# Optimization experiments

Measured on AMD Instinct MI355X. Metric: run time of the kernel, lower is better.

Reference implementation:

```python
import jax, jax.numpy as jnp
import numpy as np


def setup_inputs() -> dict:
    key = jax.random.key(0)
    x = jax.random.normal(key, (8, 192, 64, 64), dtype=jnp.float32)
    return {"x": x}


def reference(x):
    # x: [b, c, h, w]
    b, c, h, w = x.shape
    xf = x.reshape(b, c, h * w)                                   # [b, c, hw]
    # prepend global-mean token -> [b, c, T] with T = hw + 1
    xf = jnp.concatenate([xf.mean(axis=-1, keepdims=True), xf], axis=-1)
    scale = jnp.asarray(c, xf.dtype) ** -0.25                      # 1/sqrt(sqrt(c))
    qs = xf * scale
    # full T x T score matrix, as in the original module
    weight = jnp.einsum('bct,bcs->bts', qs, qs)                    # [b, T, T]
    weight = jax.nn.softmax(weight.astype(jnp.float32), axis=-1).astype(xf.dtype)
    out = jnp.einsum('bts,bcs->bct', weight, xf)                   # [b, c, T]
    return out[:, :, 0]                                            # [b, c]
```

## Files before the change

### kernel.cpp

```cpp
#include <hip/hip_runtime.h>

#define BB 8
#define CC 192
#define HWN 4096
#define SCALE2 0.07216878364870323f
#define NCHUNK 64
#define CW 64
#define PAD 193
#define NSLOT (NCHUNK + 1)

__global__ void mean_kernel(const float* __restrict__ x, float* __restrict__ m) {
    int bc = blockIdx.x;
    int t  = threadIdx.x;
    const float4* p4 = (const float4*)(x + (size_t)bc * HWN);
    float s = 0.f;
#pragma unroll
    for (int i = 0; i < 4; ++i) {
        float4 v = p4[t + i * 256];
        s += v.x + v.y + v.z + v.w;
    }
    for (int off = 32; off; off >>= 1) s += __shfl_down(s, off);
    __shared__ float sm[4];
    int wave = t >> 6, lane = t & 63;
    if (lane == 0) sm[wave] = s;
    __syncthreads();
    if (t == 0) m[bc] = (sm[0] + sm[1] + sm[2] + sm[3]) * (1.0f / HWN);
}

__global__ __launch_bounds__(256)
void fused_kernel(const float* __restrict__ x,
                  const float* __restrict__ m,
                  float2* __restrict__ pm,
                  float* __restrict__ Op) {
    const int chunk = blockIdx.x;
    const int b     = blockIdx.y;
    const int t     = threadIdx.x;

    __shared__ float tile[CW * PAD];
    __shared__ float ml[CC];
    __shared__ float scp[256];
    __shared__ float wls[CW];

    if (t < CC) ml[t] = m[b * CC + t];

    const float4* xp = (const float4*)(x + (size_t)b * CC * HWN + chunk * CW);
#pragma unroll
    for (int it = 0; it < 12; ++it) {
        int i = t + it * 256;
        int c = i >> 4, k = i & 15;
        float4 v = xp[(size_t)c * (HWN / 4) + k];
        int s = 4 * k;
        tile[(s + 0) * PAD + c] = v.x;
        tile[(s + 1) * PAD + c] = v.y;
        tile[(s + 2) * PAD + c] = v.z;
        tile[(s + 3) * PAD + c] = v.w;
    }
    __syncthreads();

    {
        int g = t >> 6, s = t & 63;
        int c0 = g * 48;
        float acc = 0.f;
#pragma unroll
        for (int c = 0; c < 48; ++c)
            acc += ml[c0 + c] * tile[s * PAD + c0 + c];
        scp[t] = acc;
    }
    __syncthreads();

    if (t < CW) {
        float sc = (scp[t] + scp[64 + t] + scp[128 + t] + scp[192 + t]) * SCALE2;
        float mx = sc;
        for (int off = 32; off; off >>= 1) mx = fmaxf(mx, __shfl_xor(mx, off));
        float w = __expf(sc - mx);
        float se = w;
        for (int off = 32; off; off >>= 1) se += __shfl_xor(se, off);
        wls[t] = w;
        if (t == 0) pm[b * NSLOT + 1 + chunk] = make_float2(mx, se);
    }
    if (chunk == 0 && t >= 64 && t < 128) {
        int u = t - 64;
        float q = ml[u] * ml[u] + ml[64 + u] * ml[64 + u] + ml[128 + u] * ml[128 + u];
        for (int off = 32; off; off >>= 1) q += __shfl_xor(q, off);
        if (u == 0) pm[b * NSLOT] = make_float2(q * SCALE2, 1.0f);
    }
    __syncthreads();

    if (t < CC) {
        float o = 0.f;
#pragma unroll 8
        for (int s = 0; s < CW; ++s)
            o += wls[s] * tile[s * PAD + t];
        Op[((size_t)b * NCHUNK + chunk) * CC + t] = o;
    }
}

__global__ void combine_kernel(const float* __restrict__ m,
                               const float2* __restrict__ pm,
                               const float* __restrict__ Op,
                               float* __restrict__ out) {
    int b = blockIdx.x;
    int t = threadIdx.x;
    __shared__ float factor[NCHUNK];
    __shared__ float sW0;

    if (t < 64) {
        float2 p1 = pm[b * NSLOT + 1 + t];
        float2 p0 = (t == 0) ? pm[b * NSLOT] : make_float2(-3.0e38f, 0.f);
        float MX = fmaxf(p1.x, p0.x);
        for (int off = 32; off; off >>= 1) MX = fmaxf(MX, __shfl_xor(MX, off));
        float z = p1.y * __expf(p1.x - MX) + p0.y * __expf(p0.x - MX);
        for (int off = 32; off; off >>= 1) z += __shfl_xor(z, off);
        float inv = 1.0f / z;
        factor[t] = __expf(p1.x - MX) * inv;
        if (t == 0) sW0 = __expf(pm[b * NSLOT].x - MX) * inv;
    }
    __syncthreads();

    if (t < CC) {
        const float* op = Op + (size_t)b * NCHUNK * CC + t;
        float o = 0.f;
#pragma unroll 16
        for (int ch = 0; ch < NCHUNK; ++ch)
            o += factor[ch] * op[(size_t)ch * CC];
        out[b * CC + t] = o + sW0 * m[b * CC + t];
    }
}

extern "C" void kernel_launch(void* const* d_in, const int* in_sizes, int n_in,
                              void* d_out, int out_size, void* d_ws, size_t ws_size,
                              hipStream_t stream) {
    const float* x = (const float*)d_in[0];
    float* out = (float*)d_out;

    float*  ws = (float*)d_ws;
    float*  m  = ws;
    float2* pm = (float2*)(ws + 1536);
    float*  Op = ws + 2592;

    mean_kernel<<<BB * CC, 256, 0, stream>>>(x, m);
    fused_kernel<<<dim3(NCHUNK, BB), 256, 0, stream>>>(x, m, pm, Op);
    combine_kernel<<<BB, 256, 0, stream>>>(m, pm, Op, out);
}
```

Baseline: 20.44 us.

## Load tiles via global_load_lds with channel-major layout and split combine across blocks

```diff
diff --git a/kernel.cpp b/kernel.cpp
--- a/kernel.cpp
+++ b/kernel.cpp
@@ -6,8 +6,12 @@
 #define SCALE2 0.07216878364870323f
 #define NCHUNK 64
 #define CW 64
-#define PAD 193
 #define NSLOT (NCHUNK + 1)
+
+#define GLOAD_LDS16(gp, lp)                                                    \
+    __builtin_amdgcn_global_load_lds(                                          \
+        (const __attribute__((address_space(1))) void*)(gp),                   \
+        (__attribute__((address_space(3))) void*)(lp), 16, 0, 0)
 
 __global__ void mean_kernel(const float* __restrict__ x, float* __restrict__ m) {
     int bc = blockIdx.x;
@@ -36,34 +40,30 @@
     const int b     = blockIdx.y;
     const int t     = threadIdx.x;
 
-    __shared__ float tile[CW * PAD];
+    __shared__ float tile[CC * CW];
     __shared__ float ml[CC];
     __shared__ float scp[256];
     __shared__ float wls[CW];
 
-    if (t < CC) ml[t] = m[b * CC + t];
-
-    const float4* xp = (const float4*)(x + (size_t)b * CC * HWN + chunk * CW);
+    const float* xb = x + (size_t)b * CC * HWN + chunk * CW;
 #pragma unroll
     for (int it = 0; it < 12; ++it) {
         int i = t + it * 256;
         int c = i >> 4, k = i & 15;
-        float4 v = xp[(size_t)c * (HWN / 4) + k];
-        int s = 4 * k;
-        tile[(s + 0) * PAD + c] = v.x;
-        tile[(s + 1) * PAD + c] = v.y;
-        tile[(s + 2) * PAD + c] = v.z;
-        tile[(s + 3) * PAD + c] = v.w;
+        const float* gsrc = xb + (size_t)c * HWN + 4 * k;
+        float* ldst = tile + 4 * (i & ~63);
+        GLOAD_LDS16(gsrc, ldst);
     }
+    if (t < CC) ml[t] = m[b * CC + t];
     __syncthreads();
 
     {
-        int g = t >> 6, s = t & 63;
-        int c0 = g * 48;
+        int grp = t >> 6, s = t & 63;
+        int c0 = grp * 48;
         float acc = 0.f;
 #pragma unroll
         for (int c = 0; c < 48; ++c)
-            acc += ml[c0 + c] * tile[s * PAD + c0 + c];
+            acc += ml[c0 + c] * tile[(c0 + c) * CW + s];
         scp[t] = acc;
     }
     __syncthreads();
@@ -88,9 +88,11 @@
 
     if (t < CC) {
         float o = 0.f;
-#pragma unroll 8
-        for (int s = 0; s < CW; ++s)
-            o += wls[s] * tile[s * PAD + t];
+#pragma unroll
+        for (int j = 0; j < CW; ++j) {
+            int s = (t + j) & 63;
+            o += wls[s] * tile[t * CW + s];
+        }
         Op[((size_t)b * NCHUNK + chunk) * CC + t] = o;
     }
 }
@@ -99,10 +101,12 @@
                                const float2* __restrict__ pm,
                                const float* __restrict__ Op,
                                float* __restrict__ out) {
-    int b = blockIdx.x;
-    int t = threadIdx.x;
+    int cg = blockIdx.x;
+    int b  = blockIdx.y;
+    int t  = threadIdx.x;
     __shared__ float factor[NCHUNK];
     __shared__ float sW0;
+    __shared__ float psum[256];
 
     if (t < 64) {
         float2 p1 = pm[b * NSLOT + 1 + t];
@@ -117,13 +121,20 @@
     }
     __syncthreads();
 
-    if (t < CC) {
-        const float* op = Op + (size_t)b * NCHUNK * CC + t;
-        float o = 0.f;
-#pragma unroll 16
-        for (int ch = 0; ch < NCHUNK; ++ch)
-            o += factor[ch] * op[(size_t)ch * CC];
-        out[b * CC + t] = o + sW0 * m[b * CC + t];
+    int q = t >> 6;
+    int c = cg * 64 + (t & 63);
+    float acc = 0.f;
+#pragma unroll
+    for (int j = 0; j < 16; ++j) {
+        int ch = q * 16 + j;
+        acc += factor[ch] * Op[((size_t)b * NCHUNK + ch) * CC + c];
+    }
+    psum[t] = acc;
+    __syncthreads();
+    if (t < 64) {
+        int cc = cg * 64 + t;
+        out[b * CC + cc] = psum[t] + psum[64 + t] + psum[128 + t] + psum[192 + t]
+                         + sW0 * m[b * CC + cc];
     }
 }
 
@@ -140,5 +151,5 @@
 
     mean_kernel<<<BB * CC, 256, 0, stream>>>(x, m);
     fused_kernel<<<dim3(NCHUNK, BB), 256, 0, stream>>>(x, m, pm, Op);
-    combine_kernel<<<BB, 256, 0, stream>>>(m, pm, Op, out);
+    combine_kernel<<<dim3(3, BB), 256, 0, stream>>>(m, pm, Op, out);
 }
```

New measurement: 19.82 us. -3.0%, faster.
